# Kernel tuning notes

Hardware: AMD Instinct MI355X
Metric: run time of the kernel (lower is better)

## Reference

```python
import jax, jax.numpy as jnp
import numpy as np

NUM_HEADS = 8


def _mha(x, w_in, b_in, w_out, b_out, nh=NUM_HEADS):
    # x: [B, L, H]; torch nn.MultiheadAttention (batch_first) self-attention
    B, L, H = x.shape
    dh = H // nh
    qkv = x @ w_in.T + b_in                      # [B, L, 3H]
    q, k, v = jnp.split(qkv, 3, axis=-1)
    def heads(t):
        return t.reshape(B, L, nh, dh).transpose(0, 2, 1, 3)  # [B, nh, L, dh]
    q, k, v = heads(q), heads(k), heads(v)
    scale = 1.0 / np.sqrt(dh)
    scores = jnp.einsum('bhqd,bhkd->bhqk', q * scale, k)      # [B, nh, L, L]
    attn = jax.nn.softmax(scores, axis=-1)
    out = jnp.einsum('bhqk,bhkd->bhqd', attn, v)               # [B, nh, L, dh]
    out = out.transpose(0, 2, 1, 3).reshape(B, L, H)
    return out @ w_out.T + b_out


def setup_inputs() -> dict:
    key = jax.random.key(0)
    ks = jax.random.split(key, 10)
    S, M, B, H = 64, 4, 128, 1024
    std = 0.02
    inp = {
        'hidden_states_combined': jax.random.normal(ks[0], (S, M, B, 1, H), jnp.float32),
        'mf_in_w': jax.random.normal(ks[1], (3 * H, H), jnp.float32) * std,
        'mf_in_b': jnp.zeros((3 * H,), jnp.float32),
        'mf_out_w': jax.random.normal(ks[2], (H, H), jnp.float32) * std,
        'mf_out_b': jnp.zeros((H,), jnp.float32),
        'sf_in_w': jax.random.normal(ks[3], (3 * H, H), jnp.float32) * std,
        'sf_in_b': jnp.zeros((3 * H,), jnp.float32),
        'sf_out_w': jax.random.normal(ks[4], (H, H), jnp.float32) * std,
        'sf_out_b': jnp.zeros((H,), jnp.float32),
        'pos_enc': jax.random.normal(ks[5], (1, S, H), jnp.float32) * std,
    }
    return inp


def reference(hidden_states_combined, mf_in_w, mf_in_b, mf_out_w, mf_out_b,
              sf_in_w, sf_in_b, sf_out_w, sf_out_b, pos_enc):
    S, M, B, _, H = hidden_states_combined.shape
    # [S, M, B, 1, H] -> [S, B, M, H] -> batch all steps together: [S*B, M, H]
    x = hidden_states_combined[:, :, :, 0, :].transpose(0, 2, 1, 3).reshape(S * B, M, H)
    fused = _mha(x, mf_in_w, mf_in_b, mf_out_w, mf_out_b)        # [S*B, M, H]
    fused = fused.mean(axis=1).reshape(S, B, H)                  # mean over models
    seq = fused.transpose(1, 0, 2) + pos_enc[:, :S, :]            # [B, S, H]
    enhanced = _mha(seq, sf_in_w, sf_in_b, sf_out_w, sf_out_b)   # [B, S, H]
    return enhanced.transpose(1, 0, 2)[:, :, None, :]             # [S, B, 1, H]
```

## Files before the change

### kernel.cpp

```cpp
#include <hip/hip_runtime.h>

typedef unsigned short u16;
typedef __attribute__((ext_vector_type(8))) short bf16x8;
typedef __attribute__((ext_vector_type(4))) float f32x4;

__device__ __forceinline__ u16 f2bf(float f) {
  unsigned u = __float_as_uint(f);
  u += 0x7FFFu + ((u >> 16) & 1u);
  return (u16)(u >> 16);
}
__device__ __forceinline__ float bf2f(u16 h) {
  return __uint_as_float(((unsigned)h) << 16);
}

#define GLOAD16(g, l) __builtin_amdgcn_global_load_lds( \
    (const __attribute__((address_space(1))) void*)(g), \
    (__attribute__((address_space(3))) void*)(l), 16, 0, 0)

__global__ __launch_bounds__(256) void cvtw4_kernel(const float* __restrict__ s0, u16* __restrict__ d0,
                                                    const float* __restrict__ s1, u16* __restrict__ d1,
                                                    const float* __restrict__ s2, u16* __restrict__ d2,
                                                    const float* __restrict__ s3, u16* __restrict__ d3) {
  int i = blockIdx.x * 256 + threadIdx.x;
  const float* s; u16* d; int off;
  if (i < 786432)       { s = s0; d = d0; off = i; }
  else if (i < 1048576) { s = s1; d = d1; off = i - 786432; }
  else if (i < 1835008) { s = s2; d = d2; off = i - 1048576; }
  else                  { s = s3; d = d3; off = i - 1835008; }
  float4 f = ((const float4*)s)[off];
  ushort4 u;
  u.x = f2bf(f.x); u.y = f2bf(f.y); u.z = f2bf(f.z); u.w = f2bf(f.w);
  ((ushort4*)d)[off] = u;
}

__global__ __launch_bounds__(256) void xcvt_kernel(const float* __restrict__ hidden,
                                                   u16* __restrict__ xb, int s0) {
  int idx = blockIdx.x * 256 + threadIdx.x;
  int h4 = idx & 255;
  int lrow = idx >> 8;
  int m = lrow & 3;
  int b = (lrow >> 2) & 127;
  int sl = lrow >> 9;
  int s = s0 + sl;
  const float4 f = *(const float4*)(hidden + (((size_t)(s * 4 + m) * 128 + b) * 1024) + h4 * 4);
  ushort4 u;
  u.x = f2bf(f.x); u.y = f2bf(f.y); u.z = f2bf(f.z); u.w = f2bf(f.w);
  *(ushort4*)(xb + (size_t)lrow * 1024 + h4 * 4) = u;
}

template <int KK>
__global__ __launch_bounds__(512, 2) void gemm4p(const u16* __restrict__ A,
                                                 const u16* __restrict__ Bw,
                                                 const float* __restrict__ bias,
                                                 u16* __restrict__ C, int N) {
  __shared__ u16 Sh[65536];
  const int t = threadIdx.x, w = t >> 6, l = t & 63;
  const int lr = l & 15, lg = l >> 4;
  const int wm = w >> 2, wn = w & 3;

  const int gx = gridDim.x;
  const int nb = gx * gridDim.y;
  const int id = blockIdx.y * gx + blockIdx.x;
  const int id2 = (id & 7) * (nb >> 3) + (id >> 3);
  const int rowBase = (id2 / gx) * 256, colBase = (id2 % gx) * 256;

  const int sslot8 = ((t & 3) ^ ((t >> 3) & 3)) * 8;
  const u16* Ag = A + (size_t)(rowBase + (t >> 2)) * KK + sslot8;
  const u16* Bg = Bw + (size_t)(colBase + (t >> 2)) * KK + sslot8;
  const size_t K128 = (size_t)128 * KK;
  const int ldsW = w * 512;

  const int fslot8 = (lg ^ ((lr >> 1) & 3)) * 8;
  const int aRowOff = (wm * 128 + lr) * 32 + fslot8;
  const int bRowOff = (wn * 64 + lr) * 32 + fslot8;

  f32x4 acc[8][4];
#pragma unroll
  for (int i = 0; i < 8; i++)
#pragma unroll
    for (int j = 0; j < 4; j++) acc[i][j] = (f32x4){0.f, 0.f, 0.f, 0.f};
  bf16x8 af[2][8], bfr[2][4];

#define STGA(tt, KH, DB) { \
    const u16* g_ = Ag + (size_t)(tt) * 64 + (KH) * 32; \
    GLOAD16(g_, Sh + ((DB) * 2 + (KH)) * 8192 + ldsW); \
    GLOAD16(g_ + K128, Sh + ((DB) * 2 + (KH)) * 8192 + 4096 + ldsW); }
#define STGB(tt, KH, DB) { \
    const u16* g_ = Bg + (size_t)(tt) * 64 + (KH) * 32; \
    GLOAD16(g_, Sh + 32768 + ((DB) * 2 + (KH)) * 8192 + ldsW); \
    GLOAD16(g_ + K128, Sh + 32768 + ((DB) * 2 + (KH)) * 8192 + 4096 + ldsW); }

#define RA8(DD, KH, BUF) { \
    const u16* sa_ = Sh + ((DD) * 2 + (KH)) * 8192 + aRowOff; \
    _Pragma("unroll") \
    for (int mi = 0; mi < 8; mi++) af[BUF][mi] = *(const bf16x8*)(sa_ + mi * 512); }
#define RB4(DD, KH, BUF) { \
    const u16* sb_ = Sh + 32768 + ((DD) * 2 + (KH)) * 8192 + bRowOff; \
    _Pragma("unroll") \
    for (int n = 0; n < 4; n++) bfr[BUF][n] = *(const bf16x8*)(sb_ + n * 512); }

#define LG(NN) asm volatile("s_waitcnt lgkmcnt(" #NN ")" ::: "memory"); \
               __builtin_amdgcn_sched_barrier(0)
#define WTC(NN) asm volatile("s_waitcnt vmcnt(" #NN ")" ::: "memory")
#define BAR asm volatile("s_barrier" ::: "memory")

#define MM32(BUF) { \
    __builtin_amdgcn_s_setprio(1); \
    _Pragma("unroll") \
    for (int mi = 0; mi < 8; mi++) { \
      _Pragma("unroll") \
      for (int n = 0; n < 4; n++) \
        acc[mi][n] = __builtin_amdgcn_mfma_f32_16x16x32_bf16( \
            af[BUF][mi], bfr[BUF][n], acc[mi][n], 0, 0, 0); \
    } \
    __builtin_amdgcn_s_setprio(0); }

  STGA(0, 0, 0); STGB(0, 0, 0);
  STGA(0, 1, 0); STGB(0, 1, 0);
  STGA(1, 0, 1); STGB(1, 0, 1);
  WTC(4);
  BAR;
  RA8(0, 0, 0); RB4(0, 0, 0);

  const int nt = KK / 64;
  for (int tt = 0; tt < nt; ++tt) {
    const int dd = tt & 1;
    RA8(dd, 1, 1); RB4(dd, 1, 1);
    if (tt + 1 < nt) { STGA(tt + 1, 1, dd ^ 1); STGB(tt + 1, 1, dd ^ 1); }
    LG(12);
    MM32(0);
    if (tt + 1 < nt) { WTC(4); }
    BAR;
    if (tt + 1 < nt) {
      RA8(dd ^ 1, 0, 0); RB4(dd ^ 1, 0, 0);
      if (tt + 2 < nt) { STGA(tt + 2, 0, dd); STGB(tt + 2, 0, dd); }
      LG(12);
    } else {
      LG(0);
    }
    MM32(1);
    if (tt + 2 < nt) { WTC(4); }
    else if (tt + 1 < nt) { WTC(0); }
    BAR;
  }
#undef MM32
#undef RB4
#undef RA8
#undef STGB
#undef STGA

  {
    const int erow0 = wm * 128 + lg * 4;
    const int ecol0 = wn * 64 + lr;
#pragma unroll
    for (int m = 0; m < 8; m++) {
#pragma unroll
      for (int n = 0; n < 4; n++) {
        const int c = ecol0 + n * 16;
        const float bv = bias[colBase + c];
#pragma unroll
        for (int r = 0; r < 4; r++) {
          const int row = erow0 + m * 16 + r;
          const int cs = (((c >> 3) ^ ((row >> 2) & 7)) << 3) | (c & 7);
          Sh[row * 256 + cs] = f2bf(acc[m][n][r] + bv);
        }
      }
    }
    BAR;
    const int g = t & 31;
    const int rsub = t >> 5;
#pragma unroll
    for (int pass = 0; pass < 16; pass++) {
      const int row = pass * 16 + rsub;
      const int gs = g ^ ((row >> 2) & 7);
      bf16x8 v = *(const bf16x8*)(Sh + row * 256 + gs * 8);
      *(bf16x8*)(&C[(size_t)(rowBase + row) * N + colBase + g * 8]) = v;
    }
  }
#undef BAR
#undef WTC
#undef LG
}

template <int MODE>
__global__ __launch_bounds__(256, 2) void gemm_fp(const u16* __restrict__ A,
                                                  const u16* __restrict__ Bw,
                                                  const float* __restrict__ bias,
                                                  void* __restrict__ Cout,
                                                  int N, int K,
                                                  const float* __restrict__ posenc) {
  __shared__ u16 SA[3][8192];
  __shared__ u16 SB[3][4096];
  const int t = threadIdx.x, w = t >> 6, l = t & 63;
  const int lr = l & 15, lg = l >> 4;
  const int wm = w >> 1, wn = w & 1;

  const int gx = gridDim.x;
  const int nb = gx * gridDim.y;
  const int id = blockIdx.y * gx + blockIdx.x;
  const int id2 = (id & 7) * (nb >> 3) + (id >> 3);
  const int rowBase = (id2 / gx) * 256, colBase = (id2 % gx) * 128;

  const int srow = l >> 2;
  const int ssl = ((l & 3) ^ (srow & 3)) * 8;
  const u16* Ag = A + (size_t)(rowBase + w * 16 + srow) * K + ssl;
  const u16* Bg = Bw + (size_t)(colBase + w * 16 + srow) * K + ssl;
  u16* const lA = &SA[0][0] + w * 512;
  u16* const lB = &SB[0][0] + w * 512;

  const int fsw = (lg ^ (lr & 3)) * 8;
  const int aoff = (wm * 128 + lr) * 32 + fsw;
  const int boff = (wn * 64 + lr) * 32 + fsw;

  f32x4 acc[8][4];
#pragma unroll
  for (int i = 0; i < 8; i++)
#pragma unroll
    for (int j = 0; j < 4; j++) acc[i][j] = (f32x4){0.f, 0.f, 0.f, 0.f};

#define STG_P0(tt, bb) do { \
    const size_t ko_ = (size_t)(tt) * 32; \
    GLOAD16(Ag + ko_,                    lA + (bb) * 8192); \
    GLOAD16(Ag + ko_ + (size_t)64 * K,   lA + (bb) * 8192 + 2048); \
    GLOAD16(Ag + ko_ + (size_t)128 * K,  lA + (bb) * 8192 + 4096); \
  } while (0)
#define STG_P1(tt, bb) do { \
    const size_t ko_ = (size_t)(tt) * 32; \
    GLOAD16(Ag + ko_ + (size_t)192 * K,  lA + (bb) * 8192 + 6144); \
    GLOAD16(Bg + ko_,                    lB + (bb) * 4096); \
    GLOAD16(Bg + ko_ + (size_t)64 * K,   lB + (bb) * 4096 + 2048); \
  } while (0)
#define FBAR asm volatile("s_barrier" ::: "memory")

  const int nt = K >> 5;
  STG_P0(0, 0); STG_P1(0, 0);
  STG_P0(1, 1); STG_P1(1, 1);
  asm volatile("s_waitcnt vmcnt(6)" ::: "memory");
  FBAR;

  int bcur = 0;
  for (int tt = 0; tt < nt; ++tt) {
    const u16* pa = &SA[bcur][0];
    const u16* pb = &SB[bcur][0];
    const int bnext = (bcur + 2 > 2) ? bcur - 1 : bcur + 2;
    bf16x8 af[4], bfr[4];

#pragma unroll
    for (int m = 0; m < 4; m++) af[m] = *(const bf16x8*)(pa + aoff + m * 512);
#pragma unroll
    for (int n = 0; n < 4; n++) bfr[n] = *(const bf16x8*)(pb + boff + n * 512);
    if (tt + 2 < nt) STG_P0(tt + 2, bnext);
    FBAR;
    asm volatile("s_waitcnt lgkmcnt(0)" ::: "memory");
    __builtin_amdgcn_sched_barrier(0);
    __builtin_amdgcn_s_setprio(1);
#pragma unroll
    for (int m = 0; m < 4; m++)
#pragma unroll
      for (int n = 0; n < 4; n++)
        acc[m][n] = __builtin_amdgcn_mfma_f32_16x16x32_bf16(af[m], bfr[n], acc[m][n], 0, 0, 0);
    __builtin_amdgcn_s_setprio(0);
    FBAR;

#pragma unroll
    for (int m = 0; m < 4; m++) af[m] = *(const bf16x8*)(pa + aoff + (m + 4) * 512);
    if (tt + 2 < nt) STG_P1(tt + 2, bnext);
    FBAR;
    asm volatile("s_waitcnt lgkmcnt(0)" ::: "memory");
    __builtin_amdgcn_sched_barrier(0);
    __builtin_amdgcn_s_setprio(1);
#pragma unroll
    for (int m = 0; m < 4; m++)
#pragma unroll
      for (int n = 0; n < 4; n++)
        acc[m + 4][n] = __builtin_amdgcn_mfma_f32_16x16x32_bf16(af[m], bfr[n], acc[m + 4][n], 0, 0, 0);
    __builtin_amdgcn_s_setprio(0);
    if (tt + 2 < nt) {
      asm volatile("s_waitcnt vmcnt(6)" ::: "memory");
    } else if (tt + 1 < nt) {
      asm volatile("s_waitcnt vmcnt(0)" ::: "memory");
    }
    FBAR;
    bcur = (bcur + 1 > 2) ? 0 : bcur + 1;
  }
#undef FBAR
#undef STG_P0
#undef STG_P1

  const int orow0 = rowBase + wm * 128 + lg * 4;
  const int ocol0 = colBase + wn * 64 + lr;
#pragma unroll
  for (int m = 0; m < 8; m++) {
#pragma unroll
    for (int n = 0; n < 4; n++) {
      const int col = ocol0 + n * 16;
      const float bv = bias[col];
#pragma unroll
      for (int r = 0; r < 4; r++) {
        const int row = orow0 + m * 16 + r;
        float v = acc[m][n][r] + bv;
        if (MODE == 1) {
          int s = row >> 7, b = row & 127;
          v += posenc[s * 1024 + col];
          ((u16*)Cout)[((size_t)(b * 64 + s)) * 1024 + col] = f2bf(v);
        } else {
          int s = row & 63, b = row >> 6;
          ((float*)Cout)[((size_t)(s * 128 + b)) * 1024 + col] = v;
        }
      }
    }
  }
}

__global__ __launch_bounds__(256) void attn1_kernel(const u16* __restrict__ qkv,
                                                    u16* __restrict__ am, int seqBase) {
  const int w = threadIdx.x >> 6, l = threadIdx.x & 63;
  const int pair = blockIdx.x * 4 + w;
  const int seq = pair >> 3, head = pair & 7;
  const int d0 = l * 2;
  const u16* base = qkv + (size_t)(seq * 4) * 3072 + head * 128 + d0;
  const float scale = 0.08838834764831845f;
  float q[4][2], k[4][2], v[4][2];
#pragma unroll
  for (int m = 0; m < 4; m++) {
    ushort2 uq = *(const ushort2*)(base + (size_t)m * 3072);
    ushort2 uk = *(const ushort2*)(base + (size_t)m * 3072 + 1024);
    ushort2 uv = *(const ushort2*)(base + (size_t)m * 3072 + 2048);
    q[m][0] = bf2f(uq.x) * scale; q[m][1] = bf2f(uq.y) * scale;
    k[m][0] = bf2f(uk.x);         k[m][1] = bf2f(uk.y);
    v[m][0] = bf2f(uv.x);         v[m][1] = bf2f(uv.y);
  }
  float sc[4][4];
#pragma unroll
  for (int i = 0; i < 4; i++)
#pragma unroll
    for (int j = 0; j < 4; j++)
      sc[i][j] = q[i][0] * k[j][0] + q[i][1] * k[j][1];
#pragma unroll
  for (int off = 32; off >= 1; off >>= 1)
#pragma unroll
    for (int i = 0; i < 4; i++)
#pragma unroll
      for (int j = 0; j < 4; j++)
        sc[i][j] += __shfl_xor(sc[i][j], off, 64);
  float pbar[4] = {0.f, 0.f, 0.f, 0.f};
#pragma unroll
  for (int i = 0; i < 4; i++) {
    float mx = fmaxf(fmaxf(sc[i][0], sc[i][1]), fmaxf(sc[i][2], sc[i][3]));
    float e0 = __expf(sc[i][0] - mx), e1 = __expf(sc[i][1] - mx);
    float e2 = __expf(sc[i][2] - mx), e3 = __expf(sc[i][3] - mx);
    float inv = 0.25f / (e0 + e1 + e2 + e3);
    pbar[0] += e0 * inv; pbar[1] += e1 * inv; pbar[2] += e2 * inv; pbar[3] += e3 * inv;
  }
  float o0 = pbar[0] * v[0][0] + pbar[1] * v[1][0] + pbar[2] * v[2][0] + pbar[3] * v[3][0];
  float o1 = pbar[0] * v[0][1] + pbar[1] * v[1][1] + pbar[2] * v[2][1] + pbar[3] * v[3][1];
  ushort2 ou; ou.x = f2bf(o0); ou.y = f2bf(o1);
  *(ushort2*)(am + (size_t)(seqBase + seq) * 1024 + head * 128 + d0) = ou;
}

__global__ __launch_bounds__(256) void attn2_kernel(const u16* __restrict__ qkv2,
                                                    u16* __restrict__ aout) {
  __shared__ u16 Qs[64 * 128];
  __shared__ u16 Ks[64 * 128];
  __shared__ u16 Vt[128 * 72];
  __shared__ u16 Ps[64 * 72];
  const int t = threadIdx.x, w = t >> 6, l = t & 63;
  const int lr = l & 15, lg = l >> 4;
  const int b = blockIdx.x >> 3, head = blockIdx.x & 7;
  const u16* qb = qkv2 + (size_t)(b * 64) * 3072 + head * 128;

#pragma unroll
  for (int c = 0; c < 4; c++) {
    int flat = c * 256 + t;
    int row = flat >> 4, sp = flat & 15;
    int sg = (sp ^ (row & 7)) * 8;
    GLOAD16(qb + (size_t)row * 3072 + sg, Qs + (c * 256 + w * 64) * 8);
    GLOAD16(qb + 1024 + (size_t)row * 3072 + sg, Ks + (c * 256 + w * 64) * 8);
  }
  const int dd = (t & 63) * 2, kb = t >> 6;
#pragma unroll
  for (int c = 0; c < 16; c++) {
    int k = c * 4 + kb;
    ushort2 vv = *(const ushort2*)(qb + 2048 + (size_t)k * 3072 + dd);
    Vt[(size_t)dd * 72 + k] = vv.x;
    Vt[(size_t)(dd + 1) * 72 + k] = vv.y;
  }
  __syncthreads();

  f32x4 sc[4];
#pragma unroll
  for (int cb = 0; cb < 4; cb++) sc[cb] = (f32x4){0.f, 0.f, 0.f, 0.f};
#pragma unroll
  for (int ks = 0; ks < 4; ks++) {
    bf16x8 aq = *(const bf16x8*)(Qs + (w * 16 + lr) * 128 + ((ks * 4 + lg) ^ (lr & 7)) * 8);
#pragma unroll
    for (int cb = 0; cb < 4; cb++) {
      bf16x8 bk = *(const bf16x8*)(Ks + (cb * 16 + lr) * 128 + ((ks * 4 + lg) ^ (lr & 7)) * 8);
      sc[cb] = __builtin_amdgcn_mfma_f32_16x16x32_bf16(aq, bk, sc[cb], 0, 0, 0);
    }
  }

  const float scale = 0.08838834764831845f;
#pragma unroll
  for (int r = 0; r < 4; r++) {
#pragma unroll
    for (int cb = 0; cb < 4; cb++) sc[cb][r] *= scale;
    float mx = fmaxf(fmaxf(sc[0][r], sc[1][r]), fmaxf(sc[2][r], sc[3][r]));
#pragma unroll
    for (int off = 1; off < 16; off <<= 1) mx = fmaxf(mx, __shfl_xor(mx, off, 64));
    float sum = 0.f;
#pragma unroll
    for (int cb = 0; cb < 4; cb++) {
      float e = __expf(sc[cb][r] - mx);
      sum += e;
      sc[cb][r] = e;
    }
#pragma unroll
    for (int off = 1; off < 16; off <<= 1) sum += __shfl_xor(sum, off, 64);
    float inv = 1.f / sum;
    int prow = w * 16 + lg * 4 + r;
#pragma unroll
    for (int cb = 0; cb < 4; cb++)
      Ps[(size_t)prow * 72 + cb * 16 + lr] = f2bf(sc[cb][r] * inv);
  }

  f32x4 o[8];
#pragma unroll
  for (int cb = 0; cb < 8; cb++) o[cb] = (f32x4){0.f, 0.f, 0.f, 0.f};
#pragma unroll
  for (int ks = 0; ks < 2; ks++) {
    bf16x8 ap = *(const bf16x8*)(Ps + (w * 16 + lr) * 72 + ks * 32 + lg * 8);
#pragma unroll
    for (int cb = 0; cb < 8; cb++) {
      bf16x8 bv = *(const bf16x8*)(Vt + (cb * 16 + lr) * 72 + ks * 32 + lg * 8);
      o[cb] = __builtin_amdgcn_mfma_f32_16x16x32_bf16(ap, bv, o[cb], 0, 0, 0);
    }
  }
#pragma unroll
  for (int cb = 0; cb < 8; cb++) {
#pragma unroll
    for (int r = 0; r < 4; r++) {
      int srow = w * 16 + lg * 4 + r;
      int d = cb * 16 + lr;
      aout[(size_t)(b * 64 + srow) * 1024 + head * 128 + d] = f2bf(o[cb][r]);
    }
  }
}

extern "C" void kernel_launch(void* const* d_in, const int* in_sizes, int n_in,
                              void* d_out, int out_size, void* d_ws, size_t ws_size,
                              hipStream_t stream) {
  const float* hidden   = (const float*)d_in[0];
  const float* mf_in_w  = (const float*)d_in[1];
  const float* mf_in_b  = (const float*)d_in[2];
  const float* mf_out_w = (const float*)d_in[3];
  const float* mf_out_b = (const float*)d_in[4];
  const float* sf_in_w  = (const float*)d_in[5];
  const float* sf_in_b  = (const float*)d_in[6];
  const float* sf_out_w = (const float*)d_in[7];
  const float* sf_out_b = (const float*)d_in[8];
  const float* pos_enc  = (const float*)d_in[9];

  char* ws = (char*)d_ws;
  u16* w_mf_in  = (u16*)(ws);
  u16* w_mf_out = (u16*)(ws + 6291456);
  u16* w_sf_in  = (u16*)(ws + 8388608);
  u16* w_sf_out = (u16*)(ws + 14680064);

  cvtw4_kernel<<<8192, 256, 0, stream>>>(mf_in_w, w_mf_in, mf_out_w, w_mf_out,
                                         sf_in_w, w_sf_in, sf_out_w, w_sf_out);

  if (ws_size >= 335544320ull) {
    u16* xfull    = (u16*)(ws + 16777216);
    u16* qkvfull  = (u16*)(ws + 83886080);
    u16* attnmean = (u16*)(ws + 285212672);
    u16* seqbuf   = (u16*)(ws + 301989888);
    u16* a2out    = (u16*)(ws + 318767104);

    xcvt_kernel<<<32768, 256, 0, stream>>>(hidden, xfull, 0);
    gemm4p<1024><<<dim3(12, 128), 512, 0, stream>>>(xfull, w_mf_in, mf_in_b, qkvfull, 3072);
    attn1_kernel<<<16384, 256, 0, stream>>>(qkvfull, attnmean, 0);

    gemm_fp<1><<<dim3(8, 32), 256, 0, stream>>>(attnmean, w_mf_out, mf_out_b, seqbuf,
                                                1024, 1024, pos_enc);
    gemm4p<1024><<<dim3(12, 32), 512, 0, stream>>>(seqbuf, w_sf_in, sf_in_b, qkvfull, 3072);
    attn2_kernel<<<1024, 256, 0, stream>>>(qkvfull, a2out);
    gemm_fp<2><<<dim3(8, 32), 256, 0, stream>>>(a2out, w_sf_out, sf_out_b, d_out,
                                                1024, 1024, nullptr);
  } else {
    u16* xchunk   = (u16*)(ws + 16777216);
    u16* qkvbuf   = (u16*)(ws + 33554432);
    u16* attnmean = (u16*)(ws + 83886080);
    u16* seqbuf   = (u16*)(ws + 100663296);
    u16* a2out    = (u16*)(ws + 117440512);

    for (int c = 0; c < 4; ++c) {
      xcvt_kernel<<<8192, 256, 0, stream>>>(hidden, xchunk, c * 16);
      gemm4p<1024><<<dim3(12, 32), 512, 0, stream>>>(xchunk, w_mf_in, mf_in_b, qkvbuf, 3072);
      attn1_kernel<<<4096, 256, 0, stream>>>(qkvbuf, attnmean, c * 2048);
    }

    gemm_fp<1><<<dim3(8, 32), 256, 0, stream>>>(attnmean, w_mf_out, mf_out_b, seqbuf,
                                                1024, 1024, pos_enc);
    gemm4p<1024><<<dim3(12, 32), 512, 0, stream>>>(seqbuf, w_sf_in, sf_in_b, qkvbuf, 3072);
    attn2_kernel<<<1024, 256, 0, stream>>>(qkvbuf, a2out);
    gemm_fp<2><<<dim3(8, 32), 256, 0, stream>>>(a2out, w_sf_out, sf_out_b, d_out,
                                                1024, 1024, nullptr);
  }
}
```

Before: 477.3 us.

## Switch QKV GEMM to 32x32x16 MFMA, direct epilogue, fuse prep kernels

The QKV projection GEMM now uses 32x32x16 bf16 MFMA tiles instead of 16x16x32. Fewer, larger matrix instructions issue per K-step, and the LDS fragment reads are re-addressed to fit. The epilogue drops the LDS-staged, swizzled, coalesced store and writes each bf16 value straight to global memory, so stores become scattered 2-byte writes. The weight conversion and input conversion kernels are merged into one launch, which removes a launch boundary.

```diff
diff --git a/kernel.cpp b/kernel.cpp
--- a/kernel.cpp
+++ b/kernel.cpp
@@ -3,6 +3,7 @@
 typedef unsigned short u16;
 typedef __attribute__((ext_vector_type(8))) short bf16x8;
 typedef __attribute__((ext_vector_type(4))) float f32x4;
+typedef __attribute__((ext_vector_type(16))) float f32x16;
 
 __device__ __forceinline__ u16 f2bf(float f) {
   unsigned u = __float_as_uint(f);
@@ -16,6 +17,37 @@
 #define GLOAD16(g, l) __builtin_amdgcn_global_load_lds( \
     (const __attribute__((address_space(1))) void*)(g), \
     (__attribute__((address_space(3))) void*)(l), 16, 0, 0)
+
+__global__ __launch_bounds__(256) void prep_kernel(const float* __restrict__ hidden,
+                                                   u16* __restrict__ xb,
+                                                   const float* __restrict__ s0, u16* __restrict__ d0,
+                                                   const float* __restrict__ s1, u16* __restrict__ d1,
+                                                   const float* __restrict__ s2, u16* __restrict__ d2,
+                                                   const float* __restrict__ s3, u16* __restrict__ d3) {
+  if (blockIdx.x < 32768) {
+    int idx = blockIdx.x * 256 + threadIdx.x;
+    int h4 = idx & 255;
+    int lrow = idx >> 8;
+    int m = lrow & 3;
+    int b = (lrow >> 2) & 127;
+    int s = lrow >> 9;
+    const float4 f = *(const float4*)(hidden + (((size_t)(s * 4 + m) * 128 + b) * 1024) + h4 * 4);
+    ushort4 u;
+    u.x = f2bf(f.x); u.y = f2bf(f.y); u.z = f2bf(f.z); u.w = f2bf(f.w);
+    *(ushort4*)(xb + (size_t)lrow * 1024 + h4 * 4) = u;
+  } else {
+    int i = (blockIdx.x - 32768) * 256 + threadIdx.x;
+    const float* s; u16* d; int off;
+    if (i < 786432)       { s = s0; d = d0; off = i; }
+    else if (i < 1048576) { s = s1; d = d1; off = i - 786432; }
+    else if (i < 1835008) { s = s2; d = d2; off = i - 1048576; }
+    else                  { s = s3; d = d3; off = i - 1835008; }
+    float4 f = ((const float4*)s)[off];
+    ushort4 u;
+    u.x = f2bf(f.x); u.y = f2bf(f.y); u.z = f2bf(f.z); u.w = f2bf(f.w);
+    ((ushort4*)d)[off] = u;
+  }
+}
 
 __global__ __launch_bounds__(256) void cvtw4_kernel(const float* __restrict__ s0, u16* __restrict__ d0,
                                                     const float* __restrict__ s1, u16* __restrict__ d1,
@@ -49,13 +81,13 @@
 }
 
 template <int KK>
-__global__ __launch_bounds__(512, 2) void gemm4p(const u16* __restrict__ A,
+__global__ __launch_bounds__(512, 2) void gemm32(const u16* __restrict__ A,
                                                  const u16* __restrict__ Bw,
                                                  const float* __restrict__ bias,
                                                  u16* __restrict__ C, int N) {
   __shared__ u16 Sh[65536];
   const int t = threadIdx.x, w = t >> 6, l = t & 63;
-  const int lr = l & 15, lg = l >> 4;
+  const int l31 = l & 31, lh = l >> 5;
   const int wm = w >> 2, wn = w & 3;
 
   const int gx = gridDim.x;
@@ -70,15 +102,17 @@
   const size_t K128 = (size_t)128 * KK;
   const int ldsW = w * 512;
 
-  const int fslot8 = (lg ^ ((lr >> 1) & 3)) * 8;
-  const int aRowOff = (wm * 128 + lr) * 32 + fslot8;
-  const int bRowOff = (wn * 64 + lr) * 32 + fslot8;
-
-  f32x4 acc[8][4];
-#pragma unroll
-  for (int i = 0; i < 8; i++)
-#pragma unroll
-    for (int j = 0; j < 4; j++) acc[i][j] = (f32x4){0.f, 0.f, 0.f, 0.f};
+  const int q = (l31 >> 1) & 3;
+  const int so0 = (lh ^ q) * 8;
+  const int so1 = ((2 + lh) ^ q) * 8;
+  const int aBase = (wm * 128 + l31) * 32;
+  const int bBase = (wn * 64 + l31) * 32;
+
+  f32x16 acc[4][2];
+#pragma unroll
+  for (int bi = 0; bi < 4; bi++)
+#pragma unroll
+    for (int bj = 0; bj < 2; bj++) acc[bi][bj] = 0.f;
   bf16x8 af[2][8], bfr[2][4];
 
 #define STGA(tt, KH, DB) { \
@@ -91,27 +125,36 @@
     GLOAD16(g_ + K128, Sh + 32768 + ((DB) * 2 + (KH)) * 8192 + 4096 + ldsW); }
 
 #define RA8(DD, KH, BUF) { \
-    const u16* sa_ = Sh + ((DD) * 2 + (KH)) * 8192 + aRowOff; \
+    const u16* sa_ = Sh + ((DD) * 2 + (KH)) * 8192 + aBase; \
     _Pragma("unroll") \
-    for (int mi = 0; mi < 8; mi++) af[BUF][mi] = *(const bf16x8*)(sa_ + mi * 512); }
+    for (int bi = 0; bi < 4; bi++) { \
+      af[BUF][bi * 2 + 0] = *(const bf16x8*)(sa_ + bi * 1024 + so0); \
+      af[BUF][bi * 2 + 1] = *(const bf16x8*)(sa_ + bi * 1024 + so1); \
+    } }
 #define RB4(DD, KH, BUF) { \
-    const u16* sb_ = Sh + 32768 + ((DD) * 2 + (KH)) * 8192 + bRowOff; \
+    const u16* sb_ = Sh + 32768 + ((DD) * 2 + (KH)) * 8192 + bBase; \
     _Pragma("unroll") \
-    for (int n = 0; n < 4; n++) bfr[BUF][n] = *(const bf16x8*)(sb_ + n * 512); }
+    for (int bj = 0; bj < 2; bj++) { \
+      bfr[BUF][bj * 2 + 0] = *(const bf16x8*)(sb_ + bj * 1024 + so0); \
+      bfr[BUF][bj * 2 + 1] = *(const bf16x8*)(sb_ + bj * 1024 + so1); \
+    } }
 
 #define LG(NN) asm volatile("s_waitcnt lgkmcnt(" #NN ")" ::: "memory"); \
                __builtin_amdgcn_sched_barrier(0)
 #define WTC(NN) asm volatile("s_waitcnt vmcnt(" #NN ")" ::: "memory")
 #define BAR asm volatile("s_barrier" ::: "memory")
 
-#define MM32(BUF) { \
+#define MM16(BUF) { \
     __builtin_amdgcn_s_setprio(1); \
     _Pragma("unroll") \
-    for (int mi = 0; mi < 8; mi++) { \
+    for (int s = 0; s < 2; s++) { \
       _Pragma("unroll") \
-      for (int n = 0; n < 4; n++) \
-        acc[mi][n] = __builtin_amdgcn_mfma_f32_16x16x32_bf16( \
-            af[BUF][mi], bfr[BUF][n], acc[mi][n], 0, 0, 0); \
+      for (int bi = 0; bi < 4; bi++) { \
+        _Pragma("unroll") \
+        for (int bj = 0; bj < 2; bj++) \
+          acc[bi][bj] = __builtin_amdgcn_mfma_f32_32x32x16_bf16( \
+              af[BUF][bi * 2 + s], bfr[BUF][bj * 2 + s], acc[bi][bj], 0, 0, 0); \
+      } \
     } \
     __builtin_amdgcn_s_setprio(0); }
 
@@ -128,7 +171,7 @@
     RA8(dd, 1, 1); RB4(dd, 1, 1);
     if (tt + 1 < nt) { STGA(tt + 1, 1, dd ^ 1); STGB(tt + 1, 1, dd ^ 1); }
     LG(12);
-    MM32(0);
+    MM16(0);
     if (tt + 1 < nt) { WTC(4); }
     BAR;
     if (tt + 1 < nt) {
@@ -138,48 +181,34 @@
     } else {
       LG(0);
     }
-    MM32(1);
+    MM16(1);
     if (tt + 2 < nt) { WTC(4); }
     else if (tt + 1 < nt) { WTC(0); }
     BAR;
   }
-#undef MM32
+#undef MM16
+#undef BAR
+#undef WTC
+#undef LG
 #undef RB4
 #undef RA8
 #undef STGB
 #undef STGA
 
-  {
-    const int erow0 = wm * 128 + lg * 4;
-    const int ecol0 = wn * 64 + lr;
-#pragma unroll
-    for (int m = 0; m < 8; m++) {
-#pragma unroll
-      for (int n = 0; n < 4; n++) {
-        const int c = ecol0 + n * 16;
-        const float bv = bias[colBase + c];
-#pragma unroll
-        for (int r = 0; r < 4; r++) {
-          const int row = erow0 + m * 16 + r;
-          const int cs = (((c >> 3) ^ ((row >> 2) & 7)) << 3) | (c & 7);
-          Sh[row * 256 + cs] = f2bf(acc[m][n][r] + bv);
-        }
+  const int orow0 = rowBase + wm * 128 + lh * 4;
+  const int ocol = colBase + wn * 64 + l31;
+#pragma unroll
+  for (int bj = 0; bj < 2; bj++) {
+    const float bv = bias[ocol + bj * 32];
+#pragma unroll
+    for (int bi = 0; bi < 4; bi++) {
+#pragma unroll
+      for (int r = 0; r < 16; r++) {
+        const int row = orow0 + bi * 32 + (r & 3) + 8 * (r >> 2);
+        C[(size_t)row * N + ocol + bj * 32] = f2bf(acc[bi][bj][r] + bv);
       }
     }
-    BAR;
-    const int g = t & 31;
-    const int rsub = t >> 5;
-#pragma unroll
-    for (int pass = 0; pass < 16; pass++) {
-      const int row = pass * 16 + rsub;
-      const int gs = g ^ ((row >> 2) & 7);
-      bf16x8 v = *(const bf16x8*)(Sh + row * 256 + gs * 8);
-      *(bf16x8*)(&C[(size_t)(rowBase + row) * N + colBase + g * 8]) = v;
-    }
-  }
-#undef BAR
-#undef WTC
-#undef LG
+  }
 }
 
 template <int MODE>
@@ -467,9 +496,6 @@
   u16* w_sf_in  = (u16*)(ws + 8388608);
   u16* w_sf_out = (u16*)(ws + 14680064);
 
-  cvtw4_kernel<<<8192, 256, 0, stream>>>(mf_in_w, w_mf_in, mf_out_w, w_mf_out,
-                                         sf_in_w, w_sf_in, sf_out_w, w_sf_out);
-
   if (ws_size >= 335544320ull) {
     u16* xfull    = (u16*)(ws + 16777216);
     u16* qkvfull  = (u16*)(ws + 83886080);
@@ -477,13 +503,15 @@
     u16* seqbuf   = (u16*)(ws + 301989888);
     u16* a2out    = (u16*)(ws + 318767104);
 
-    xcvt_kernel<<<32768, 256, 0, stream>>>(hidden, xfull, 0);
-    gemm4p<1024><<<dim3(12, 128), 512, 0, stream>>>(xfull, w_mf_in, mf_in_b, qkvfull, 3072);
+    prep_kernel<<<40960, 256, 0, stream>>>(hidden, xfull,
+                                           mf_in_w, w_mf_in, mf_out_w, w_mf_out,
+                                           sf_in_w, w_sf_in, sf_out_w, w_sf_out);
+    gemm32<1024><<<dim3(12, 128), 512, 0, stream>>>(xfull, w_mf_in, mf_in_b, qkvfull, 3072);
     attn1_kernel<<<16384, 256, 0, stream>>>(qkvfull, attnmean, 0);
 
     gemm_fp<1><<<dim3(8, 32), 256, 0, stream>>>(attnmean, w_mf_out, mf_out_b, seqbuf,
                                                 1024, 1024, pos_enc);
-    gemm4p<1024><<<dim3(12, 32), 512, 0, stream>>>(seqbuf, w_sf_in, sf_in_b, qkvfull, 3072);
+    gemm32<1024><<<dim3(12, 32), 512, 0, stream>>>(seqbuf, w_sf_in, sf_in_b, qkvfull, 3072);
     attn2_kernel<<<1024, 256, 0, stream>>>(qkvfull, a2out);
     gemm_fp<2><<<dim3(8, 32), 256, 0, stream>>>(a2out, w_sf_out, sf_out_b, d_out,
                                                 1024, 1024, nullptr);
@@ -494,15 +522,17 @@
     u16* seqbuf   = (u16*)(ws + 100663296);
     u16* a2out    = (u16*)(ws + 117440512);
 
+    cvtw4_kernel<<<8192, 256, 0, stream>>>(mf_in_w, w_mf_in, mf_out_w, w_mf_out,
+                                           sf_in_w, w_sf_in, sf_out_w, w_sf_out);
     for (int c = 0; c < 4; ++c) {
       xcvt_kernel<<<8192, 256, 0, stream>>>(hidden, xchunk, c * 16);
-      gemm4p<1024><<<dim3(12, 32), 512, 0, stream>>>(xchunk, w_mf_in, mf_in_b, qkvbuf, 3072);
+      gemm32<1024><<<dim3(12, 32), 512, 0, stream>>>(xchunk, w_mf_in, mf_in_b, qkvbuf, 3072);
       attn1_kernel<<<4096, 256, 0, stream>>>(qkvbuf, attnmean, c * 2048);
     }
 
     gemm_fp<1><<<dim3(8, 32), 256, 0, stream>>>(attnmean, w_mf_out, mf_out_b, seqbuf,
                                                 1024, 1024, pos_enc);
-    gemm4p<1024><<<dim3(12, 32), 512, 0, stream>>>(seqbuf, w_sf_in, sf_in_b, qkvbuf, 3072);
+    gemm32<1024><<<dim3(12, 32), 512, 0, stream>>>(seqbuf, w_sf_in, sf_in_b, qkvbuf, 3072);
     attn2_kernel<<<1024, 256, 0, stream>>>(qkvbuf, a2out);
     gemm_fp<2><<<dim3(8, 32), 256, 0, stream>>>(a2out, w_sf_out, sf_out_b, d_out,
                                                 1024, 1024, nullptr);
```

Result: slower. 507.6 us (+6.4%).
